# Optimization experiments

Hardware: AMD Instinct MI355X
Metric: run time of the kernel (lower is better)

The kernel has to match this reference:

```python
import jax, jax.numpy as jnp
import numpy as np

NW = 64        # n_waveshapers
CE = 128       # control_embedding_size
W = 16         # shaping_fn_size (width)
OC = 1         # out_channels
EPS = 1e-5
SLOPE = 0.01   # LeakyReLU negative slope


def _layer_norm_c(x, g, b):
    # layer norm over channel axis of [B, C, T] (TimeDistributedLayerNorm)
    mu = jnp.mean(x, axis=1, keepdims=True)
    var = jnp.var(x, axis=1, keepdims=True)
    xn = (x - mu) * jax.lax.rsqrt(var + EPS)
    return xn * g[None, :, None] + b[None, :, None]


def _linear_interp(x, out_len):
    # torch F.interpolate(mode='linear', align_corners=False) on [B, C, L]
    L = x.shape[-1]
    scale = L / out_len
    pos = (jnp.arange(out_len, dtype=x.dtype) + 0.5) * scale - 0.5
    pos = jnp.clip(pos, 0.0, L - 1)
    i0 = jnp.floor(pos).astype(jnp.int32)
    i1 = jnp.minimum(i0 + 1, L - 1)
    frac = (pos - i0.astype(x.dtype))
    return x[..., i0] * (1.0 - frac) + x[..., i1] * frac


def setup_inputs() -> dict:
    key = jax.random.key(0)
    ks = jax.random.split(key, 32)
    B, T, TC = 4, 65536, 1024
    s_ce = 1.0 / np.sqrt(CE)
    inp = {
        'exciter': jax.random.normal(ks[0], (B, NW, T), jnp.float32),
        'control_embedding': jax.random.normal(ks[1], (B, CE, TC), jnp.float32),
        # TimeDistributedMLP (depth=4): three CE->CE convs + final CE->4*NW
        'mlp_w0': jax.random.normal(ks[2], (CE, CE), jnp.float32) * s_ce,
        'mlp_b0': jnp.zeros((CE,), jnp.float32),
        'ln0_g': jnp.ones((CE,), jnp.float32),
        'ln0_b': jnp.zeros((CE,), jnp.float32),
        'mlp_w1': jax.random.normal(ks[3], (CE, CE), jnp.float32) * s_ce,
        'mlp_b1': jnp.zeros((CE,), jnp.float32),
        'ln1_g': jnp.ones((CE,), jnp.float32),
        'ln1_b': jnp.zeros((CE,), jnp.float32),
        'mlp_w2': jax.random.normal(ks[4], (CE, CE), jnp.float32) * s_ce,
        'mlp_b2': jnp.zeros((CE,), jnp.float32),
        'ln2_g': jnp.ones((CE,), jnp.float32),
        'ln2_b': jnp.zeros((CE,), jnp.float32),
        'mlp_w3': jax.random.normal(ks[5], (4 * NW, CE), jnp.float32) * s_ce,
        'mlp_b3': jnp.zeros((4 * NW,), jnp.float32),
        # TrainableNonlinearity: input_scale + grouped k=1 convs (per-channel MLPs)
        'input_scale': jax.random.normal(ks[6], (1, NW, 1), jnp.float32) * 10.0,
        'sf_w0': jax.random.normal(ks[7], (NW, W), jnp.float32),            # 1 -> W per group
        'sf_b0': jnp.zeros((NW, W), jnp.float32),
        'sf_w1': jax.random.normal(ks[8], (NW, W, W), jnp.float32) / np.sqrt(W),  # W -> W per group
        'sf_b1': jnp.zeros((NW, W), jnp.float32),
        'sf_w2': jax.random.normal(ks[9], (NW, W), jnp.float32) / np.sqrt(W),     # W -> 1 per group
        'sf_b2': jnp.zeros((NW,), jnp.float32),
        # mixer conv1d NW -> OC, k=1
        'mix_w': jax.random.normal(ks[10], (OC, NW), jnp.float32) / np.sqrt(NW),
        'mix_b': jnp.zeros((OC,), jnp.float32),
    }
    return inp


def reference(exciter, control_embedding,
              mlp_w0, mlp_b0, ln0_g, ln0_b,
              mlp_w1, mlp_b1, ln1_g, ln1_b,
              mlp_w2, mlp_b2, ln2_g, ln2_b,
              mlp_w3, mlp_b3,
              input_scale, sf_w0, sf_b0, sf_w1, sf_b1, sf_w2, sf_b2,
              mix_w, mix_b):
    T = exciter.shape[-1]

    # --- TimeDistributedMLP: (Conv1x1 -> LN(channels) -> LeakyReLU) x3 -> Conv1x1
    h = jnp.einsum('bct,oc->bot', control_embedding, mlp_w0) + mlp_b0[None, :, None]
    h = jax.nn.leaky_relu(_layer_norm_c(h, ln0_g, ln0_b), SLOPE)
    h = jnp.einsum('bct,oc->bot', h, mlp_w1) + mlp_b1[None, :, None]
    h = jax.nn.leaky_relu(_layer_norm_c(h, ln1_g, ln1_b), SLOPE)
    h = jnp.einsum('bct,oc->bot', h, mlp_w2) + mlp_b2[None, :, None]
    h = jax.nn.leaky_relu(_layer_norm_c(h, ln2_g, ln2_b), SLOPE)
    film = jnp.einsum('bct,oc->bot', h, mlp_w3) + mlp_b3[None, :, None]  # [B, 4*NW, TC]

    # upsample control params to audio rate
    film = _linear_interp(film, T)  # [B, 4*NW, T]
    gamma_i, beta_i, gamma_n, beta_n = jnp.split(film, 4, axis=1)

    # FiLM waveshaping index
    x = gamma_i * exciter + beta_i  # [B, NW, T]

    # TrainableNonlinearity: per-channel 1->W->W->1 MLP, Sine activations
    x = input_scale * x
    h0 = jnp.sin(x[:, :, None, :] * sf_w0[None, :, :, None] + sf_b0[None, :, :, None])  # [B,NW,W,T]
    h1 = jnp.sin(jnp.einsum('bcit,coi->bcot', h0, sf_w1) + sf_b1[None, :, :, None])     # [B,NW,W,T]
    x = jnp.sin(jnp.einsum('bcit,ci->bct', h1, sf_w2) + sf_b2[None, :, None])           # [B,NW,T]

    # FiLM normalising coeff
    x = gamma_n * x + beta_n

    # nearest upsample x4 then 1x1 mixer conv
    x = jnp.repeat(x, 4, axis=-1)  # [B, NW, 4T]
    out = jnp.einsum('bct,oc->bot', x, mix_w) + mix_b[None, :, None]  # [B, OC, 4T]
    return out
```

## Files before the change

### kernel.cpp

```cpp
#include <hip/hip_runtime.h>
#include <stdint.h>

#define NB 4
#define NWS 64
#define TT 65536
#define TCC 1024
#define CEE 128
#define WW 16

#define INV2PI 0.15915494309189535f

#define OFF_FILM  0
#define OFF_W0S   (OFF_FILM + NB*256*TCC)
#define OFF_B0S   (OFF_W0S + 1024)
#define OFF_B1S   (OFF_B0S + 1024)
#define OFF_B2S   (OFF_B1S + 1024)
#define OFF_MIX   (OFF_B2S + 64)
#define OFF_AFRAG (OFF_MIX + 64)
#define OFF_PART  (OFF_AFRAG + 16384)

typedef _Float16 half4_t __attribute__((ext_vector_type(4)));
typedef float f32x4_t __attribute__((ext_vector_type(4)));

__device__ __forceinline__ float sinrev(float r) {
#if __has_builtin(__builtin_amdgcn_fractf) && __has_builtin(__builtin_amdgcn_sinf)
  return __builtin_amdgcn_sinf(__builtin_amdgcn_fractf(r));
#else
  float fr = r - floorf(r);
  return __sinf(fr * 6.283185307179586f);
#endif
}

__global__ __launch_bounds__(256) void k_prep(
    const float* __restrict__ iscale,
    const float* __restrict__ w0, const float* __restrict__ b0,
    const float* __restrict__ w1, const float* __restrict__ b1,
    const float* __restrict__ w2, const float* __restrict__ b2,
    const float* __restrict__ mixw,
    float* __restrict__ ws) {
  int i = blockIdx.x * 256 + threadIdx.x;
  if (i < NWS * WW) {
    int n = i / WW;
    ws[OFF_W0S + i] = w0[i] * iscale[n] * INV2PI;
    ws[OFF_B0S + i] = b0[i] * INV2PI;
    ws[OFF_B1S + i] = b1[i] * INV2PI;
  }
  if (i < NWS) {
    ws[OFF_B2S + i] = b2[i] * INV2PI;
    ws[OFF_MIX + i] = mixw[i];
  }
  if (i < NWS * 64) {
    int n = i >> 6, l = i & 63;
    int m = l & 15, k0 = (l >> 4) * 4;
    union { uint2 u; half4_t h; } cv;
    #pragma unroll
    for (int j = 0; j < 4; ++j)
      cv.h[j] = (_Float16)(w1[(n * 16 + m) * 16 + k0 + j] * INV2PI);
    union { uint2 u; half4_t h; } c2;
    #pragma unroll
    for (int j = 0; j < 4; ++j)
      c2.h[j] = (_Float16)(w2[n * 16 + k0 + j] * INV2PI);
    uint4 o; o.x = cv.u.x; o.y = cv.u.y; o.z = c2.u.x; o.w = c2.u.y;
    ((uint4*)(ws + OFF_AFRAG))[i] = o;
  }
}

#define MCOLS 8
__global__ __launch_bounds__(256) void k_mlp(
    const float* __restrict__ ce,
    const float* __restrict__ w0, const float* __restrict__ b0,
    const float* __restrict__ g0, const float* __restrict__ e0,
    const float* __restrict__ w1, const float* __restrict__ b1,
    const float* __restrict__ g1, const float* __restrict__ e1,
    const float* __restrict__ w2, const float* __restrict__ b2,
    const float* __restrict__ g2, const float* __restrict__ e2,
    const float* __restrict__ w3, const float* __restrict__ b3,
    float* __restrict__ film) {
  const int tid = threadIdx.x;
  const int o = tid & 127;
  const int h = tid >> 7;
  const int wvid = tid >> 6;
  const int bx = blockIdx.x;
  const int b = bx >> 7;
  const int tc0 = (bx & 127) * MCOLS;

  __shared__ float wlds[128 * 65];
  __shared__ __align__(16) float xa[CEE * MCOLS];
  __shared__ __align__(16) float xb[CEE * MCOLS];
  __shared__ float red[4][2][4];
  __shared__ float stat[2][MCOLS];

  if (tid < 128) {
    const float* src = ce + ((size_t)(b * CEE + tid)) * TCC + tc0;
    *(float4*)(xa + tid * MCOLS) = *(const float4*)src;
    *(float4*)(xa + tid * MCOLS + 4) = *(const float4*)(src + 4);
  }

  float* xin = xa; float* xout = xb;
  const float* Wp[3] = {w0, w1, w2};
  const float* Bp[3] = {b0, b1, b2};
  const float* Gp[3] = {g0, g1, g2};
  const float* Ep[3] = {e0, e1, e2};

  for (int L = 0; L < 3; ++L) {
    float acc[4];
    float bias = Bp[L][o];
    #pragma unroll
    for (int cc = 0; cc < 4; ++cc) acc[cc] = bias;

    for (int half = 0; half < 2; ++half) {
      __syncthreads();
      const float* wsrc = Wp[L] + half * 64;
      for (int i = tid; i < 4096; i += 256) {
        int oo = i >> 5, cc2 = (i & 31) * 2;
        float2 wv = *(const float2*)(wsrc + (size_t)oo * CEE + cc2);
        wlds[oo * 65 + cc2] = wv.x;
        wlds[oo * 65 + cc2 + 1] = wv.y;
      }
      __syncthreads();
      const float* xcol = xin + half * 64 * MCOLS + h * 4;
      const float* wr = wlds + o * 65;
      #pragma unroll 8
      for (int c = 0; c < 64; ++c) {
        float w = wr[c];
        float4 xv = *(const float4*)(xcol + c * MCOLS);
        acc[0] = fmaf(w, xv.x, acc[0]); acc[1] = fmaf(w, xv.y, acc[1]);
        acc[2] = fmaf(w, xv.z, acc[2]); acc[3] = fmaf(w, xv.w, acc[3]);
      }
    }

    float s[4], q[4];
    #pragma unroll
    for (int cc = 0; cc < 4; ++cc) { s[cc] = acc[cc]; q[cc] = acc[cc] * acc[cc]; }
    #pragma unroll
    for (int m = 1; m < 64; m <<= 1) {
      #pragma unroll
      for (int cc = 0; cc < 4; ++cc) {
        s[cc] += __shfl_xor(s[cc], m, 64);
        q[cc] += __shfl_xor(q[cc], m, 64);
      }
    }
    if ((tid & 63) == 0) {
      #pragma unroll
      for (int cc = 0; cc < 4; ++cc) { red[wvid][0][cc] = s[cc]; red[wvid][1][cc] = q[cc]; }
    }
    __syncthreads();
    if (tid < MCOLS) {
      int hh = tid >> 2, cc = tid & 3;
      float st = red[2 * hh][0][cc] + red[2 * hh + 1][0][cc];
      float qt = red[2 * hh][1][cc] + red[2 * hh + 1][1][cc];
      float mu = st * (1.0f / CEE);
      float var = qt * (1.0f / CEE) - mu * mu;
      stat[0][tid] = mu;
      stat[1][tid] = rsqrtf(var + 1e-5f);
    }
    __syncthreads();
    float g = Gp[L][o], e = Ep[L][o];
    #pragma unroll
    for (int cc = 0; cc < 4; ++cc) {
      int col = h * 4 + cc;
      float v = (acc[cc] - stat[0][col]) * stat[1][col] * g + e;
      v = fmaxf(v, 0.01f * v);
      xout[o * MCOLS + col] = v;
    }
    float* tmp = xin; xin = xout; xout = tmp;
  }

  for (int hh = 0; hh < 2; ++hh) {
    float acc[4];
    float bias = b3[hh * 128 + o];
    #pragma unroll
    for (int cc = 0; cc < 4; ++cc) acc[cc] = bias;
    for (int half = 0; half < 2; ++half) {
      __syncthreads();
      const float* wsrc = w3 + (size_t)hh * 128 * CEE + half * 64;
      for (int i = tid; i < 4096; i += 256) {
        int oo = i >> 5, cc2 = (i & 31) * 2;
        float2 wv = *(const float2*)(wsrc + (size_t)oo * CEE + cc2);
        wlds[oo * 65 + cc2] = wv.x;
        wlds[oo * 65 + cc2 + 1] = wv.y;
      }
      __syncthreads();
      const float* xcol = xin + half * 64 * MCOLS + h * 4;
      const float* wr = wlds + o * 65;
      #pragma unroll 8
      for (int c = 0; c < 64; ++c) {
        float w = wr[c];
        float4 xv = *(const float4*)(xcol + c * MCOLS);
        acc[0] = fmaf(w, xv.x, acc[0]); acc[1] = fmaf(w, xv.y, acc[1]);
        acc[2] = fmaf(w, xv.z, acc[2]); acc[3] = fmaf(w, xv.w, acc[3]);
      }
    }
    float* dst = film + ((size_t)(b * 256 + hh * 128 + o)) * TCC + tc0 + h * 4;
    *(float4*)dst = *(float4*)acc;
  }
}

__global__ __launch_bounds__(256, 8) void k_shape(
    const float* __restrict__ exciter,
    const float* __restrict__ ws,
    float* __restrict__ part) {
  const int tid = threadIdx.x;
  const int lane = tid & 63;
  const int wv = tid >> 6;
  const int bx = blockIdx.x;
  const int blk = bx & 255;
  const int b = (bx >> 8) & 3;
  const int half = bx >> 10;
  const int n0 = half * 32;
  const int t0_blk = blk * 256;
  const int tcbase = blk * 4 - 1;

  __shared__ float FLraw[32 * 24];
  __shared__ float FLp[32 * 36];
  __shared__ float Sraw[8], Spair[12];
  __shared__ __align__(16) float W0s[32 * 16], B0s[32 * 16], B1s[32 * 16];
  __shared__ float B2s[32], MWs[32];

  for (int i = tid; i < 512; i += 256) {
    W0s[i] = ws[OFF_W0S + n0 * 16 + i];
    B0s[i] = ws[OFF_B0S + n0 * 16 + i];
    B1s[i] = ws[OFF_B1S + n0 * 16 + i];
  }
  if (tid < 32) {
    B2s[tid] = ws[OFF_B2S + n0 + tid];
    MWs[tid] = ws[OFF_MIX + n0 + tid];
  }
  for (int i = tid; i < 768; i += 256) {
    int n = i / 24, r = i - n * 24, p = r / 6, j = r - p * 6;
    int tc = tcbase + j; tc = tc < 0 ? 0 : (tc > 1023 ? 1023 : tc);
    FLraw[i] = ws[OFF_FILM + ((size_t)(b * 256 + p * 64 + n0 + n)) * TCC + tc];
  }
  __syncthreads();
  for (int i = tid; i < 576; i += 256) {
    int n = i / 18, r = i - n * 18, p = r / 6, j = r - p * 6;
    float v = FLraw[n * 24 + p * 6 + j];
    float vn = (j < 5) ? FLraw[n * 24 + p * 6 + j + 1] : v;
    float sc = (p == 2) ? MWs[n] : 1.0f;
    FLp[n * 36 + p * 12 + 2 * j] = v * sc;
    FLp[n * 36 + p * 12 + 2 * j + 1] = (vn - v) * sc;
  }
  if (tid < 6) {
    float s = 0.0f;
    for (int n = 0; n < 32; ++n) s += MWs[n] * FLraw[n * 24 + 18 + tid];
    Sraw[tid] = s;
  }
  __syncthreads();
  if (tid < 6) {
    Spair[2 * tid] = Sraw[tid];
    Spair[2 * tid + 1] = (tid < 5) ? Sraw[tid + 1] - Sraw[tid] : 0.0f;
  }
  __syncthreads();

  const int t_own = t0_blk + wv * 64 + lane;
  float pos = ((float)t_own + 0.5f) * (1.0f / 64.0f) - 0.5f;
  pos = fminf(fmaxf(pos, 0.0f), 1023.0f);
  float fi = floorf(pos);
  int i0 = (int)fi;
  const float frac = pos - fi;
  const int j0 = i0 - tcbase;

  const int quad = lane >> 4;
  const int l16 = lane & 15;

  float acc = 0.0f;
  const float* excp = exciter + ((size_t)(b * NWS + n0)) * TT + t_own;
  const uint4* afp = (const uint4*)(ws + OFF_AFRAG) + (size_t)n0 * 64 + lane;

  f32x4_t czero; czero[0] = 0.f; czero[1] = 0.f; czero[2] = 0.f; czero[3] = 0.f;

  float ev = excp[0];
  uint4 af = afp[0];
  for (int n = 0; n < 32; ++n) {
    float ev_n = 0.f; uint4 af_n = af;
    if (n < 31) {
      ev_n = excp[(size_t)(n + 1) * TT];
      af_n = afp[(n + 1) * 64];
    }
    const float* fp = FLp + n * 36 + 2 * j0;
    float2 gp = *(const float2*)(fp);
    float2 bp = *(const float2*)(fp + 12);
    float2 np = *(const float2*)(fp + 24);
    float gi = fmaf(gp.y, frac, gp.x);
    float bi = fmaf(bp.y, frac, bp.x);
    float gnp = fmaf(np.y, frac, np.x);
    float x = fmaf(gi, ev, bi);

    f32x4_t w0f = *(const f32x4_t*)(W0s + n * 16 + quad * 4);
    f32x4_t b0f = *(const f32x4_t*)(B0s + n * 16 + quad * 4);
    f32x4_t b1f = *(const f32x4_t*)(B1s + n * 16 + quad * 4);
    float b2v = B2s[n];
    half4_t a1, a2;
    { union { uint2 u; half4_t h; } cv; cv.u.x = af.x; cv.u.y = af.y; a1 = cv.h; }
    { union { uint2 u; half4_t h; } cv; cv.u.x = af.z; cv.u.y = af.w; a2 = cv.h; }

    float yown = 0.0f;
    #pragma unroll
    for (int g = 0; g < 4; ++g) {
      float xg = __shfl(x, g * 16 + l16, 64);
      half4_t bf1;
      #pragma unroll
      for (int k = 0; k < 4; ++k)
        bf1[k] = (_Float16)sinrev(fmaf(xg, w0f[k], b0f[k]));
      f32x4_t d1 = __builtin_amdgcn_mfma_f32_16x16x16f16(a1, bf1, b1f, 0, 0, 0);
      half4_t bf2;
      #pragma unroll
      for (int k = 0; k < 4; ++k)
        bf2[k] = (_Float16)sinrev(d1[k]);
      f32x4_t d2 = __builtin_amdgcn_mfma_f32_16x16x16f16(a2, bf2, czero, 0, 0, 0);
      yown = (quad == g) ? d2[0] : yown;
    }
    float z = sinrev(yown + b2v);
    acc = fmaf(gnp, z, acc);
    ev = ev_n; af = af_n;
  }
  float2 sp = *(const float2*)(Spair + 2 * j0);
  part[((size_t)(half * NB + b)) * TT + t_own] = acc + fmaf(sp.y, frac, sp.x);
}

__global__ __launch_bounds__(256) void k_mix(
    const float* __restrict__ part,
    const float* __restrict__ mixb,
    float* __restrict__ out) {
  int idx = blockIdx.x * 256 + threadIdx.x;
  float m = mixb[0];
  float4 a = ((const float4*)part)[idx];
  float4 c = ((const float4*)(part + NB * TT))[idx];
  float4* o = (float4*)(out + (size_t)idx * 16);
  float s0 = a.x + c.x + m, s1 = a.y + c.y + m, s2 = a.z + c.z + m, s3 = a.w + c.w + m;
  o[0] = make_float4(s0, s0, s0, s0);
  o[1] = make_float4(s1, s1, s1, s1);
  o[2] = make_float4(s2, s2, s2, s2);
  o[3] = make_float4(s3, s3, s3, s3);
}

extern "C" void kernel_launch(void* const* d_in, const int* in_sizes, int n_in,
                              void* d_out, int out_size, void* d_ws, size_t ws_size,
                              hipStream_t stream) {
  const float* exciter = (const float*)d_in[0];
  const float* ce      = (const float*)d_in[1];
  const float* w0  = (const float*)d_in[2];
  const float* b0  = (const float*)d_in[3];
  const float* g0  = (const float*)d_in[4];
  const float* e0  = (const float*)d_in[5];
  const float* w1  = (const float*)d_in[6];
  const float* b1  = (const float*)d_in[7];
  const float* g1  = (const float*)d_in[8];
  const float* e1  = (const float*)d_in[9];
  const float* w2  = (const float*)d_in[10];
  const float* b2  = (const float*)d_in[11];
  const float* g2  = (const float*)d_in[12];
  const float* e2  = (const float*)d_in[13];
  const float* w3  = (const float*)d_in[14];
  const float* b3  = (const float*)d_in[15];
  const float* iscale = (const float*)d_in[16];
  const float* sw0 = (const float*)d_in[17];
  const float* sb0 = (const float*)d_in[18];
  const float* sw1 = (const float*)d_in[19];
  const float* sb1 = (const float*)d_in[20];
  const float* sw2 = (const float*)d_in[21];
  const float* sb2 = (const float*)d_in[22];
  const float* mixw = (const float*)d_in[23];
  const float* mixb = (const float*)d_in[24];

  float* ws = (float*)d_ws;

  hipLaunchKernelGGL(k_prep, dim3(16), dim3(256), 0, stream,
                     iscale, sw0, sb0, sw1, sb1, sw2, sb2, mixw, ws);
  hipLaunchKernelGGL(k_mlp, dim3(512), dim3(256), 0, stream,
                     ce, w0, b0, g0, e0, w1, b1, g1, e1, w2, b2, g2, e2, w3, b3,
                     ws + OFF_FILM);
  hipLaunchKernelGGL(k_shape, dim3(2048), dim3(256), 0, stream,
                     exciter, ws, ws + OFF_PART);
  hipLaunchKernelGGL(k_mix, dim3(256), dim3(256), 0, stream,
                     ws + OFF_PART, mixb, (float*)d_out);
}
```

Measured before the change: 258.7 us.

## Fold prep into MLP kernel, split shaping into quarters, precompute mixed beta sum

Removes the separate prep kernel by having the first 16 MLP blocks write the shaping weights. The MLP kernel also computes the mix-weighted sum of beta_n per control frame, so the shaping kernel no longer reduces it. The shaping kernel now splits the waveshapers into four groups of 16 (4096 blocks instead of 2048) for more parallelism, uses a packed FiLM layout in LDS, and converts to fp16 with packed cvt_pkrtz. The mix kernel then reads and sums four partial buffers instead of two, which adds partial-buffer traffic.

New measurement: 249.4 us. 3.6% less time.

```diff
diff --git a/kernel.cpp b/kernel.cpp
--- a/kernel.cpp
+++ b/kernel.cpp
@@ -11,16 +11,20 @@
 #define INV2PI 0.15915494309189535f
 
 #define OFF_FILM  0
-#define OFF_W0S   (OFF_FILM + NB*256*TCC)
+#define OFF_SB    (OFF_FILM + NB*256*TCC)
+#define OFF_W0S   (OFF_SB + NB*TCC)
 #define OFF_B0S   (OFF_W0S + 1024)
 #define OFF_B1S   (OFF_B0S + 1024)
 #define OFF_B2S   (OFF_B1S + 1024)
-#define OFF_MIX   (OFF_B2S + 64)
-#define OFF_AFRAG (OFF_MIX + 64)
+#define OFF_AFRAG (OFF_B2S + 64)
 #define OFF_PART  (OFF_AFRAG + 16384)
 
 typedef _Float16 half4_t __attribute__((ext_vector_type(4)));
+typedef _Float16 half2_t __attribute__((ext_vector_type(2)));
+typedef __fp16 fp16x2_t __attribute__((ext_vector_type(2)));
 typedef float f32x4_t __attribute__((ext_vector_type(4)));
+
+union H4 { half4_t h4; half2_t h2[2]; fp16x2_t f2[2]; uint2 u; };
 
 __device__ __forceinline__ float sinrev(float r) {
 #if __has_builtin(__builtin_amdgcn_fractf) && __has_builtin(__builtin_amdgcn_sinf)
@@ -29,40 +33,6 @@
   float fr = r - floorf(r);
   return __sinf(fr * 6.283185307179586f);
 #endif
-}
-
-__global__ __launch_bounds__(256) void k_prep(
-    const float* __restrict__ iscale,
-    const float* __restrict__ w0, const float* __restrict__ b0,
-    const float* __restrict__ w1, const float* __restrict__ b1,
-    const float* __restrict__ w2, const float* __restrict__ b2,
-    const float* __restrict__ mixw,
-    float* __restrict__ ws) {
-  int i = blockIdx.x * 256 + threadIdx.x;
-  if (i < NWS * WW) {
-    int n = i / WW;
-    ws[OFF_W0S + i] = w0[i] * iscale[n] * INV2PI;
-    ws[OFF_B0S + i] = b0[i] * INV2PI;
-    ws[OFF_B1S + i] = b1[i] * INV2PI;
-  }
-  if (i < NWS) {
-    ws[OFF_B2S + i] = b2[i] * INV2PI;
-    ws[OFF_MIX + i] = mixw[i];
-  }
-  if (i < NWS * 64) {
-    int n = i >> 6, l = i & 63;
-    int m = l & 15, k0 = (l >> 4) * 4;
-    union { uint2 u; half4_t h; } cv;
-    #pragma unroll
-    for (int j = 0; j < 4; ++j)
-      cv.h[j] = (_Float16)(w1[(n * 16 + m) * 16 + k0 + j] * INV2PI);
-    union { uint2 u; half4_t h; } c2;
-    #pragma unroll
-    for (int j = 0; j < 4; ++j)
-      c2.h[j] = (_Float16)(w2[n * 16 + k0 + j] * INV2PI);
-    uint4 o; o.x = cv.u.x; o.y = cv.u.y; o.z = c2.u.x; o.w = c2.u.y;
-    ((uint4*)(ws + OFF_AFRAG))[i] = o;
-  }
 }
 
 #define MCOLS 8
@@ -75,14 +45,44 @@
     const float* __restrict__ w2, const float* __restrict__ b2,
     const float* __restrict__ g2, const float* __restrict__ e2,
     const float* __restrict__ w3, const float* __restrict__ b3,
-    float* __restrict__ film) {
+    const float* __restrict__ iscale,
+    const float* __restrict__ sw0, const float* __restrict__ sb0,
+    const float* __restrict__ sw1, const float* __restrict__ sb1,
+    const float* __restrict__ sw2, const float* __restrict__ sb2,
+    const float* __restrict__ mixw,
+    float* __restrict__ ws) {
   const int tid = threadIdx.x;
+  const int bx = blockIdx.x;
+
+  if (bx < 16) {
+    int i = bx * 256 + tid;
+    if (i < NWS * WW) {
+      int n = i / WW;
+      ws[OFF_W0S + i] = sw0[i] * iscale[n] * INV2PI;
+      ws[OFF_B0S + i] = sb0[i] * INV2PI;
+      ws[OFF_B1S + i] = sb1[i] * INV2PI;
+    }
+    if (i < NWS) ws[OFF_B2S + i] = sb2[i] * INV2PI;
+    {
+      int n = i >> 6, l = i & 63;
+      int m = l & 15, k0 = (l >> 4) * 4;
+      H4 a1, a2;
+      #pragma unroll
+      for (int j = 0; j < 4; ++j) {
+        a1.h4[j] = (_Float16)(sw1[(n * 16 + m) * 16 + k0 + j] * INV2PI);
+        a2.h4[j] = (_Float16)(sw2[n * 16 + k0 + j] * INV2PI);
+      }
+      uint4 o; o.x = a1.u.x; o.y = a1.u.y; o.z = a2.u.x; o.w = a2.u.y;
+      ((uint4*)(ws + OFF_AFRAG))[i] = o;
+    }
+  }
+
   const int o = tid & 127;
   const int h = tid >> 7;
   const int wvid = tid >> 6;
-  const int bx = blockIdx.x;
   const int b = bx >> 7;
   const int tc0 = (bx & 127) * MCOLS;
+  float* film = ws + OFF_FILM;
 
   __shared__ float wlds[128 * 65];
   __shared__ __align__(16) float xa[CEE * MCOLS];
@@ -193,12 +193,31 @@
     }
     float* dst = film + ((size_t)(b * 256 + hh * 128 + o)) * TCC + tc0 + h * 4;
     *(float4*)dst = *(float4*)acc;
+
+    if (hh == 1 && ((tid >> 6) & 1)) {
+      int n = o - 64;
+      float mwn = mixw[n];
+      float sv[4];
+      #pragma unroll
+      for (int cc = 0; cc < 4; ++cc) sv[cc] = mwn * acc[cc];
+      #pragma unroll
+      for (int m = 1; m < 64; m <<= 1) {
+        #pragma unroll
+        for (int cc = 0; cc < 4; ++cc) sv[cc] += __shfl_xor(sv[cc], m, 64);
+      }
+      if ((tid & 63) == 0) {
+        #pragma unroll
+        for (int cc = 0; cc < 4; ++cc)
+          ws[OFF_SB + b * TCC + tc0 + h * 4 + cc] = sv[cc];
+      }
+    }
   }
 }
 
 __global__ __launch_bounds__(256, 8) void k_shape(
     const float* __restrict__ exciter,
     const float* __restrict__ ws,
+    const float* __restrict__ mixw,
     float* __restrict__ part) {
   const int tid = threadIdx.x;
   const int lane = tid & 63;
@@ -206,49 +225,43 @@
   const int bx = blockIdx.x;
   const int blk = bx & 255;
   const int b = (bx >> 8) & 3;
-  const int half = bx >> 10;
-  const int n0 = half * 32;
+  const int quarter = bx >> 10;
+  const int n0 = quarter * 16;
   const int t0_blk = blk * 256;
   const int tcbase = blk * 4 - 1;
 
-  __shared__ float FLraw[32 * 24];
-  __shared__ float FLp[32 * 36];
-  __shared__ float Sraw[8], Spair[12];
-  __shared__ __align__(16) float W0s[32 * 16], B0s[32 * 16], B1s[32 * 16];
-  __shared__ float B2s[32], MWs[32];
-
-  for (int i = tid; i < 512; i += 256) {
-    W0s[i] = ws[OFF_W0S + n0 * 16 + i];
-    B0s[i] = ws[OFF_B0S + n0 * 16 + i];
-    B1s[i] = ws[OFF_B1S + n0 * 16 + i];
-  }
-  if (tid < 32) {
-    B2s[tid] = ws[OFF_B2S + n0 + tid];
-    MWs[tid] = ws[OFF_MIX + n0 + tid];
-  }
-  for (int i = tid; i < 768; i += 256) {
-    int n = i / 24, r = i - n * 24, p = r / 6, j = r - p * 6;
+  __shared__ __align__(16) float FLp[16 * 48];
+  __shared__ float Spair[12];
+  __shared__ __align__(16) float W0s[16 * 16], B0s[16 * 16], B1s[16 * 16];
+  __shared__ float B2s[16];
+
+  if (tid < 16 * 16) {
+    W0s[tid] = ws[OFF_W0S + n0 * 16 + tid];
+    B0s[tid] = ws[OFF_B0S + n0 * 16 + tid];
+    B1s[tid] = ws[OFF_B1S + n0 * 16 + tid];
+  }
+  if (tid < 16) B2s[tid] = ws[OFF_B2S + n0 + tid];
+  if (tid < 96) {
+    int n = tid / 6, j = tid - n * 6;
     int tc = tcbase + j; tc = tc < 0 ? 0 : (tc > 1023 ? 1023 : tc);
-    FLraw[i] = ws[OFF_FILM + ((size_t)(b * 256 + p * 64 + n0 + n)) * TCC + tc];
-  }
-  __syncthreads();
-  for (int i = tid; i < 576; i += 256) {
-    int n = i / 18, r = i - n * 18, p = r / 6, j = r - p * 6;
-    float v = FLraw[n * 24 + p * 6 + j];
-    float vn = (j < 5) ? FLraw[n * 24 + p * 6 + j + 1] : v;
-    float sc = (p == 2) ? MWs[n] : 1.0f;
-    FLp[n * 36 + p * 12 + 2 * j] = v * sc;
-    FLp[n * 36 + p * 12 + 2 * j + 1] = (vn - v) * sc;
-  }
-  if (tid < 6) {
-    float s = 0.0f;
-    for (int n = 0; n < 32; ++n) s += MWs[n] * FLraw[n * 24 + 18 + tid];
-    Sraw[tid] = s;
-  }
-  __syncthreads();
-  if (tid < 6) {
-    Spair[2 * tid] = Sraw[tid];
-    Spair[2 * tid + 1] = (tid < 5) ? Sraw[tid + 1] - Sraw[tid] : 0.0f;
+    int tcn = tcbase + j + 1; tcn = tcn < 0 ? 0 : (tcn > 1023 ? 1023 : tcn);
+    const float* fb = ws + OFF_FILM + ((size_t)(b * 256 + n0 + n)) * TCC;
+    float g_v = fb[tc], g_n = fb[tcn];
+    float b_v = fb[64 * TCC + tc], b_n = fb[64 * TCC + tcn];
+    float n_v = fb[128 * TCC + tc], n_n = fb[128 * TCC + tcn];
+    float mwn = mixw[n0 + n];
+    float* d = FLp + n * 48 + j * 8;
+    d[0] = g_v; d[1] = g_n - g_v;
+    d[2] = b_v; d[3] = b_n - b_v;
+    d[4] = n_v * mwn; d[5] = (n_n - n_v) * mwn;
+  }
+  if (tid >= 96 && tid < 102 && quarter == 0) {
+    int j = tid - 96;
+    int tc = tcbase + j; tc = tc < 0 ? 0 : (tc > 1023 ? 1023 : tc);
+    int tcn = tcbase + j + 1; tcn = tcn < 0 ? 0 : (tcn > 1023 ? 1023 : tcn);
+    float s0 = ws[OFF_SB + b * TCC + tc];
+    float s1 = ws[OFF_SB + b * TCC + tcn];
+    Spair[2 * j] = s0; Spair[2 * j + 1] = s1 - s0;
   }
   __syncthreads();
 
@@ -271,18 +284,17 @@
 
   float ev = excp[0];
   uint4 af = afp[0];
-  for (int n = 0; n < 32; ++n) {
+  for (int n = 0; n < 16; ++n) {
     float ev_n = 0.f; uint4 af_n = af;
-    if (n < 31) {
+    if (n < 15) {
       ev_n = excp[(size_t)(n + 1) * TT];
       af_n = afp[(n + 1) * 64];
     }
-    const float* fp = FLp + n * 36 + 2 * j0;
-    float2 gp = *(const float2*)(fp);
-    float2 bp = *(const float2*)(fp + 12);
-    float2 np = *(const float2*)(fp + 24);
-    float gi = fmaf(gp.y, frac, gp.x);
-    float bi = fmaf(bp.y, frac, bp.x);
+    const float* fp = FLp + n * 48 + j0 * 8;
+    float4 gb = *(const float4*)(fp);
+    float2 np = *(const float2*)(fp + 4);
+    float gi = fmaf(gb.y, frac, gb.x);
+    float bi = fmaf(gb.w, frac, gb.z);
     float gnp = fmaf(np.y, frac, np.x);
     float x = fmaf(gi, ev, bi);
 
@@ -290,32 +302,41 @@
     f32x4_t b0f = *(const f32x4_t*)(B0s + n * 16 + quad * 4);
     f32x4_t b1f = *(const f32x4_t*)(B1s + n * 16 + quad * 4);
     float b2v = B2s[n];
-    half4_t a1, a2;
-    { union { uint2 u; half4_t h; } cv; cv.u.x = af.x; cv.u.y = af.y; a1 = cv.h; }
-    { union { uint2 u; half4_t h; } cv; cv.u.x = af.z; cv.u.y = af.w; a2 = cv.h; }
+    H4 a1, a2;
+    a1.u.x = af.x; a1.u.y = af.y;
+    a2.u.x = af.z; a2.u.y = af.w;
 
     float yown = 0.0f;
     #pragma unroll
     for (int g = 0; g < 4; ++g) {
       float xg = __shfl(x, g * 16 + l16, 64);
-      half4_t bf1;
-      #pragma unroll
-      for (int k = 0; k < 4; ++k)
-        bf1[k] = (_Float16)sinrev(fmaf(xg, w0f[k], b0f[k]));
-      f32x4_t d1 = __builtin_amdgcn_mfma_f32_16x16x16f16(a1, bf1, b1f, 0, 0, 0);
-      half4_t bf2;
-      #pragma unroll
-      for (int k = 0; k < 4; ++k)
-        bf2[k] = (_Float16)sinrev(d1[k]);
-      f32x4_t d2 = __builtin_amdgcn_mfma_f32_16x16x16f16(a2, bf2, czero, 0, 0, 0);
+      float s0 = sinrev(fmaf(xg, w0f[0], b0f[0]));
+      float s1 = sinrev(fmaf(xg, w0f[1], b0f[1]));
+      float s2 = sinrev(fmaf(xg, w0f[2], b0f[2]));
+      float s3 = sinrev(fmaf(xg, w0f[3], b0f[3]));
+      H4 bf1;
+      bf1.f2[0] = __builtin_amdgcn_cvt_pkrtz(s0, s1);
+      bf1.f2[1] = __builtin_amdgcn_cvt_pkrtz(s2, s3);
+      f32x4_t d1 = __builtin_amdgcn_mfma_f32_16x16x16f16(a1.h4, bf1.h4, b1f, 0, 0, 0);
+      float u0 = sinrev(d1[0]);
+      float u1 = sinrev(d1[1]);
+      float u2 = sinrev(d1[2]);
+      float u3 = sinrev(d1[3]);
+      H4 bf2;
+      bf2.f2[0] = __builtin_amdgcn_cvt_pkrtz(u0, u1);
+      bf2.f2[1] = __builtin_amdgcn_cvt_pkrtz(u2, u3);
+      f32x4_t d2 = __builtin_amdgcn_mfma_f32_16x16x16f16(a2.h4, bf2.h4, czero, 0, 0, 0);
       yown = (quad == g) ? d2[0] : yown;
     }
     float z = sinrev(yown + b2v);
     acc = fmaf(gnp, z, acc);
     ev = ev_n; af = af_n;
   }
-  float2 sp = *(const float2*)(Spair + 2 * j0);
-  part[((size_t)(half * NB + b)) * TT + t_own] = acc + fmaf(sp.y, frac, sp.x);
+  if (quarter == 0) {
+    float2 sp = *(const float2*)(Spair + 2 * j0);
+    acc += fmaf(sp.y, frac, sp.x);
+  }
+  part[((size_t)(quarter * NB + b)) * TT + t_own] = acc;
 }
 
 __global__ __launch_bounds__(256) void k_mix(
@@ -325,9 +346,14 @@
   int idx = blockIdx.x * 256 + threadIdx.x;
   float m = mixb[0];
   float4 a = ((const float4*)part)[idx];
-  float4 c = ((const float4*)(part + NB * TT))[idx];
+  float4 c = ((const float4*)(part + (size_t)NB * TT))[idx];
+  float4 d = ((const float4*)(part + (size_t)2 * NB * TT))[idx];
+  float4 e = ((const float4*)(part + (size_t)3 * NB * TT))[idx];
   float4* o = (float4*)(out + (size_t)idx * 16);
-  float s0 = a.x + c.x + m, s1 = a.y + c.y + m, s2 = a.z + c.z + m, s3 = a.w + c.w + m;
+  float s0 = a.x + c.x + d.x + e.x + m;
+  float s1 = a.y + c.y + d.y + e.y + m;
+  float s2 = a.z + c.z + d.z + e.z + m;
+  float s3 = a.w + c.w + d.w + e.w + m;
   o[0] = make_float4(s0, s0, s0, s0);
   o[1] = make_float4(s1, s1, s1, s1);
   o[2] = make_float4(s2, s2, s2, s2);
@@ -365,13 +391,11 @@
 
   float* ws = (float*)d_ws;
 
-  hipLaunchKernelGGL(k_prep, dim3(16), dim3(256), 0, stream,
-                     iscale, sw0, sb0, sw1, sb1, sw2, sb2, mixw, ws);
   hipLaunchKernelGGL(k_mlp, dim3(512), dim3(256), 0, stream,
                      ce, w0, b0, g0, e0, w1, b1, g1, e1, w2, b2, g2, e2, w3, b3,
-                     ws + OFF_FILM);
-  hipLaunchKernelGGL(k_shape, dim3(2048), dim3(256), 0, stream,
-                     exciter, ws, ws + OFF_PART);
+                     iscale, sw0, sb0, sw1, sb1, sw2, sb2, mixw, ws);
+  hipLaunchKernelGGL(k_shape, dim3(4096), dim3(256), 0, stream,
+                     exciter, ws, mixw, ws + OFF_PART);
   hipLaunchKernelGGL(k_mix, dim3(256), dim3(256), 0, stream,
                      ws + OFF_PART, mixb, (float*)d_out);
 }
```
